# Optimization experiments

Hardware: AMD Instinct MI355X
Metric: run time of the kernel (lower is better)

The kernel has to match this reference:

```python
import jax, jax.numpy as jnp
import numpy as np

EMBED_DIM = 1024
NUM_HEADS = 16
HEAD_DIM = EMBED_DIM // NUM_HEADS


def setup_inputs() -> dict:
    key = jax.random.key(0)
    ks = jax.random.split(key, 5)
    B, N, D = 4, 2048, EMBED_DIM
    scale = 1.0 / np.sqrt(D)
    return {
        "x": jax.random.normal(ks[0], (B, N, D), dtype=jnp.float32),
        "w_qkv": jax.random.normal(ks[1], (D, 3 * D), dtype=jnp.float32) * scale,
        "b_qkv": jnp.zeros((3 * D,), dtype=jnp.float32),
        "w_proj": jax.random.normal(ks[2], (D, D), dtype=jnp.float32) * scale,
        "b_proj": jnp.zeros((D,), dtype=jnp.float32),
    }


def reference(x, w_qkv, b_qkv, w_proj, b_proj):
    B, N, D = x.shape
    H, Hd = NUM_HEADS, HEAD_DIM
    qkv = x @ w_qkv + b_qkv                      # [B, N, 3D]
    # 'b n (three h d) -> three b h n d'
    qkv = qkv.reshape(B, N, 3, H, Hd).transpose(2, 0, 3, 1, 4)
    q, k, v = qkv[0], qkv[1], qkv[2]             # each [B, H, N, Hd]
    scores = jnp.einsum('bhnd,bhmd->bhnm', q, k) / np.sqrt(Hd)
    probs = jax.nn.softmax(scores, axis=-1)      # dropout is identity in eval
    out = jnp.einsum('bhnm,bhmd->bhnd', probs, v)
    out = out.transpose(0, 2, 1, 3).reshape(B, N, D)  # 'b h n d -> b n (h d)'
    return out @ w_proj + b_proj
```

## Files before the change

kernel.cpp:

```cpp
#include <hip/hip_runtime.h>
#include <hip/hip_bf16.h>

#define DEVI __device__ __forceinline__

typedef float f32x4  __attribute__((ext_vector_type(4)));
typedef float f32x16 __attribute__((ext_vector_type(16)));
typedef short bf16x8 __attribute__((ext_vector_type(8)));
typedef int   i32x4  __attribute__((ext_vector_type(4)));

constexpr int BATCH = 4;
constexpr int SEQ   = 2048;
constexpr int DIM   = 1024;
constexpr int NH    = 16;
constexpr int HD    = 64;
constexpr int TD    = 3 * DIM;
constexpr int MTOT  = BATCH * SEQ;

constexpr float QSCALE = 0.125f * 1.44269504f;

DEVI unsigned short f2bf(float f) {
    __hip_bfloat16 h = __float2bfloat16(f);
    return *reinterpret_cast<unsigned short*>(&h);
}

DEVI void gload_lds16(const unsigned short* gsrc, unsigned short* ldst) {
    __builtin_amdgcn_global_load_lds(
        (const __attribute__((address_space(1))) void*)gsrc,
        (__attribute__((address_space(3))) void*)ldst,
        16, 0, 0);
}

__global__ void cvt_kernel(const float* __restrict__ in, unsigned short* __restrict__ out, int n4) {
    int i = blockIdx.x * blockDim.x + threadIdx.x;
    int stride = gridDim.x * blockDim.x;
    for (; i < n4; i += stride) {
        float4 v = reinterpret_cast<const float4*>(in)[i];
        ushort4 o;
        o.x = f2bf(v.x); o.y = f2bf(v.y); o.z = f2bf(v.z); o.w = f2bf(v.w);
        reinterpret_cast<ushort4*>(out)[i] = o;
    }
}

__global__ void transp_kernel(const float* __restrict__ in, unsigned short* __restrict__ out, int R, int C) {
    __shared__ float tile[32][33];
    int c0 = blockIdx.x * 32, r0 = blockIdx.y * 32;
    int tx = threadIdx.x, ty = threadIdx.y;
#pragma unroll
    for (int i = 0; i < 32; i += 8)
        tile[ty + i][tx] = in[(long)(r0 + ty + i) * C + c0 + tx];
    __syncthreads();
#pragma unroll
    for (int i = 0; i < 32; i += 8)
        out[(long)(c0 + ty + i) * R + r0 + tx] = f2bf(tile[tx][ty + i]);
}

template <bool OUT_BF16>
__global__ __launch_bounds__(256) void gemm_bt_kernel(
    const unsigned short* __restrict__ A,
    const unsigned short* __restrict__ Bt,
    const float* __restrict__ bias,
    void* __restrict__ Cout,
    int M, int Nn, int K, int scale_ncols, float scl)
{
    __shared__ unsigned short As[128 * 32];
    __shared__ unsigned short Bs[128 * 32];

    const int t  = threadIdx.x;
    const int l  = t & 63;
    const int w  = t >> 6;
    const int wr = w >> 1, wc = w & 1;
    const int tr = blockIdx.y, tc = blockIdx.x;
    const int lrow = l & 15, lk = l >> 4;

    f32x4 acc[4][4] = {};

    const int r0  = t >> 2;
    const int ch0 = t & 3;
    const long arow_base = (long)(tr * 128) * K;
    const long brow_base = (long)(tc * 128) * K;

    const int nk = K >> 5;
    for (int kt = 0; kt < nk; ++kt) {
        const int kb = kt * 32;
        gload_lds16(A  + arow_base + (long)r0 * K        + kb + ch0 * 8, &As[t * 8]);
        gload_lds16(A  + arow_base + (long)(r0 + 64) * K + kb + ch0 * 8, &As[(t + 256) * 8]);
        gload_lds16(Bt + brow_base + (long)r0 * K        + kb + ch0 * 8, &Bs[t * 8]);
        gload_lds16(Bt + brow_base + (long)(r0 + 64) * K + kb + ch0 * 8, &Bs[(t + 256) * 8]);
        __syncthreads();

        bf16x8 a[4], bb[4];
#pragma unroll
        for (int mi = 0; mi < 4; ++mi)
            a[mi] = *(const bf16x8*)&As[(wr * 64 + mi * 16 + lrow) * 32 + lk * 8];
#pragma unroll
        for (int ni = 0; ni < 4; ++ni)
            bb[ni] = *(const bf16x8*)&Bs[(wc * 64 + ni * 16 + lrow) * 32 + lk * 8];
#pragma unroll
        for (int mi = 0; mi < 4; ++mi)
#pragma unroll
            for (int ni = 0; ni < 4; ++ni)
                acc[mi][ni] = __builtin_amdgcn_mfma_f32_16x16x32_bf16(a[mi], bb[ni], acc[mi][ni], 0, 0, 0);
        __syncthreads();
    }

    const int row_base = tr * 128 + wr * 64;
    const int col_base = tc * 128 + wc * 64;
    const float mult = (col_base < scale_ncols) ? scl : 1.0f;
    float bv[4];
#pragma unroll
    for (int ni = 0; ni < 4; ++ni) bv[ni] = bias[col_base + ni * 16 + lrow];

#pragma unroll
    for (int mi = 0; mi < 4; ++mi)
#pragma unroll
        for (int ni = 0; ni < 4; ++ni)
#pragma unroll
            for (int r = 0; r < 4; ++r) {
                int row = row_base + mi * 16 + lk * 4 + r;
                int col = col_base + ni * 16 + lrow;
                float v = (acc[mi][ni][r] + bv[ni]) * mult;
                if (OUT_BF16) ((unsigned short*)Cout)[(long)row * Nn + col] = f2bf(v);
                else          ((float*)Cout)[(long)row * Nn + col] = v;
            }
}

__global__ __launch_bounds__(256, 2) void attn_kernel(
    const unsigned short* __restrict__ qkv,
    unsigned short* __restrict__ aout)
{
    constexpr int KVB  = 64;
    constexpr int PADW = 72;
    __shared__ unsigned short Ks[KVB * PADW];
    __shared__ unsigned short VsT[HD * PADW];

    const int t = threadIdx.x;
    const int l = t & 63;
    const int w = t >> 6;
    const int ln = l & 31;
    const int hi = l >> 5;

    const int b  = blockIdx.y >> 4;
    const int h  = blockIdx.y & 15;
    const int q0 = blockIdx.x * 128 + w * 32;

    bf16x8 bq[4];
    {
        const long qrow = (long)(b * SEQ + q0 + ln) * TD + h * HD;
#pragma unroll
        for (int s = 0; s < 4; ++s)
            bq[s] = *(const bf16x8*)&qkv[qrow + s * 16 + hi * 8];
    }

    f32x16 o[2];
#pragma unroll
    for (int i = 0; i < 16; ++i) { o[0][i] = 0.f; o[1][i] = 0.f; }
    float mrun = -1e30f, lsum = 0.f;

    const long kbase = (long)(b * SEQ) * TD + DIM + h * HD;
    const long vbase = (long)(b * SEQ) * TD + 2 * DIM + h * HD;

    const int krow = t & 63, kc0 = (t >> 6) * 8;
    const int vch = t >> 5, vrp = t & 31;

    i32x4 kr0, kr1, vr0, vr1;

#define LOAD_TILE(m0) do {                                                     \
        const unsigned short* kp = &qkv[kbase + (long)((m0) + krow) * TD + kc0]; \
        kr0 = *(const i32x4*)kp;                                               \
        kr1 = *(const i32x4*)(kp + 32);                                        \
        const unsigned short* vp = &qkv[vbase + (long)((m0) + 2 * vrp) * TD + vch * 8]; \
        vr0 = *(const i32x4*)vp;                                               \
        vr1 = *(const i32x4*)(vp + TD);                                        \
    } while (0)

#define WRITE_TILE() do {                                                      \
        *(i32x4*)&Ks[krow * PADW + kc0]      = kr0;                            \
        *(i32x4*)&Ks[krow * PADW + kc0 + 32] = kr1;                            \
        const unsigned short* u0 = (const unsigned short*)&vr0;                \
        const unsigned short* u1 = (const unsigned short*)&vr1;                \
        unsigned int* V32 = (unsigned int*)VsT;                                \
        _Pragma("unroll")                                                      \
        for (int j = 0; j < 8; ++j) {                                          \
            unsigned int word = (unsigned int)u0[j] | ((unsigned int)u1[j] << 16); \
            V32[(vch * 8 + j) * 36 + vrp] = word;                              \
        }                                                                      \
    } while (0)

    LOAD_TILE(0);
    WRITE_TILE();
    __syncthreads();

    for (int m0 = 0; m0 < SEQ; m0 += KVB) {
        const int mn = (m0 + KVB) & (SEQ - 1);
        LOAD_TILE(mn);

        f32x16 sv[2];
        __builtin_amdgcn_s_setprio(1);
#pragma unroll
        for (int f = 0; f < 2; ++f) {
            f32x16 acc = {};
#pragma unroll
            for (int s = 0; s < 4; ++s) {
                bf16x8 ak = *(const bf16x8*)&Ks[(f * 32 + ln) * PADW + s * 16 + hi * 8];
                acc = __builtin_amdgcn_mfma_f32_32x32x16_bf16(ak, bq[s], acc, 0, 0, 0);
            }
            sv[f] = acc;
        }
        __builtin_amdgcn_s_setprio(0);

        float vm = sv[0][0];
#pragma unroll
        for (int i = 1; i < 16; ++i) vm = fmaxf(vm, sv[0][i]);
#pragma unroll
        for (int i = 0; i < 16; ++i) vm = fmaxf(vm, sv[1][i]);
        vm = fmaxf(vm, __shfl_xor(vm, 32));

        if (!__all(vm <= mrun + 8.f)) {
            float mnew = fmaxf(mrun, vm);
            float sc = exp2f(mrun - mnew);
            mrun = mnew;
            lsum *= sc;
#pragma unroll
            for (int f = 0; f < 2; ++f)
#pragma unroll
                for (int i = 0; i < 16; ++i) o[f][i] *= sc;
        }

        float ps = 0.f;
#pragma unroll
        for (int f = 0; f < 2; ++f)
#pragma unroll
            for (int i = 0; i < 16; ++i) {
                float p = exp2f(sv[f][i] - mrun);
                sv[f][i] = p;
                ps += p;
            }
        ps += __shfl_xor(ps, 32);
        lsum += ps;

        bf16x8 pb[4];
#pragma unroll
        for (int ks = 0; ks < 4; ++ks) {
            const int f = ks >> 1, base = (ks & 1) * 8;
            unsigned x0, x1, y0, y1;
            asm("v_cvt_pk_bf16_f32 %0, %1, %2" : "=v"(x0) : "v"(sv[f][base + 0]), "v"(sv[f][base + 1]));
            asm("v_cvt_pk_bf16_f32 %0, %1, %2" : "=v"(x1) : "v"(sv[f][base + 2]), "v"(sv[f][base + 3]));
            asm("v_cvt_pk_bf16_f32 %0, %1, %2" : "=v"(y0) : "v"(sv[f][base + 4]), "v"(sv[f][base + 5]));
            asm("v_cvt_pk_bf16_f32 %0, %1, %2" : "=v"(y1) : "v"(sv[f][base + 6]), "v"(sv[f][base + 7]));
            asm("v_permlane32_swap_b32 %0, %1" : "+v"(x0), "+v"(y0));
            asm("v_permlane32_swap_b32 %0, %1" : "+v"(x1), "+v"(y1));
            union { unsigned u[4]; bf16x8 v; } pu;
            pu.u[0] = x0; pu.u[1] = x1; pu.u[2] = y0; pu.u[3] = y1;
            pb[ks] = pu.v;
        }

        __builtin_amdgcn_s_setprio(1);
#pragma unroll
        for (int f2 = 0; f2 < 2; ++f2)
#pragma unroll
            for (int ks = 0; ks < 4; ++ks) {
                bf16x8 av = *(const bf16x8*)&VsT[(f2 * 32 + ln) * PADW + ks * 16 + hi * 8];
                o[f2] = __builtin_amdgcn_mfma_f32_32x32x16_bf16(av, pb[ks], o[f2], 0, 0, 0);
            }
        __builtin_amdgcn_s_setprio(0);

        __syncthreads();
        WRITE_TILE();
        __syncthreads();
    }

#undef LOAD_TILE
#undef WRITE_TILE

    float inv = 1.0f / lsum;
    const long orow = (long)(b * SEQ + q0 + ln);
#pragma unroll
    for (int f2 = 0; f2 < 2; ++f2)
#pragma unroll
        for (int g = 0; g < 4; ++g) {
            ushort4 st;
            st.x = f2bf(o[f2][4 * g + 0] * inv);
            st.y = f2bf(o[f2][4 * g + 1] * inv);
            st.z = f2bf(o[f2][4 * g + 2] * inv);
            st.w = f2bf(o[f2][4 * g + 3] * inv);
            *(ushort4*)&aout[orow * DIM + h * HD + f2 * 32 + 8 * g + 4 * hi] = st;
        }
}

extern "C" void kernel_launch(void* const* d_in, const int* in_sizes, int n_in,
                              void* d_out, int out_size, void* d_ws, size_t ws_size,
                              hipStream_t stream)
{
    const float* x      = (const float*)d_in[0];
    const float* w_qkv  = (const float*)d_in[1];
    const float* b_qkv  = (const float*)d_in[2];
    const float* w_proj = (const float*)d_in[3];
    const float* b_proj = (const float*)d_in[4];
    float* out = (float*)d_out;

    unsigned short* x_bf   = (unsigned short*)d_ws;
    unsigned short* wqkvT  = x_bf   + (size_t)MTOT * DIM;
    unsigned short* wprojT = wqkvT  + (size_t)TD * DIM;
    unsigned short* qkv    = wprojT + (size_t)DIM * DIM;
    unsigned short* attn   = qkv    + (size_t)MTOT * TD;

    cvt_kernel<<<2048, 256, 0, stream>>>(x, x_bf, MTOT * DIM / 4);
    dim3 tb(32, 8);
    transp_kernel<<<dim3(TD / 32, DIM / 32), tb, 0, stream>>>(w_qkv, wqkvT, DIM, TD);
    transp_kernel<<<dim3(DIM / 32, DIM / 32), tb, 0, stream>>>(w_proj, wprojT, DIM, DIM);

    gemm_bt_kernel<true><<<dim3(TD / 128, MTOT / 128), 256, 0, stream>>>(
        x_bf, wqkvT, b_qkv, qkv, MTOT, TD, DIM, DIM, QSCALE);

    attn_kernel<<<dim3(SEQ / 128, BATCH * NH), 256, 0, stream>>>(qkv, attn);

    gemm_bt_kernel<false><<<dim3(DIM / 128, MTOT / 128), 256, 0, stream>>>(
        attn, wprojT, b_proj, out, MTOT, DIM, DIM, 0, 1.0f);
}
```

Measured before the change: 237.6 us.

## Double-buffer attention K/V tiles, swizzle blocks across XCDs, tree-reduce softmax

The attention kernel now uses two LDS buffers for K and V^T, so the next tile is written into the spare buffer and only one barrier per iteration is needed instead of two. Both the GEMM and attention kernels remap block indices so consecutive tiles land on the same XCD, which is meant to improve L2 reuse. The row max and row sum are rebuilt as balanced trees to shorten the dependency chains, and the attention kernel's min-2-blocks launch bound is dropped. Doubling LDS and relaxing the occupancy hint may lower occupancy. The attention swizzle hardcodes a 16x128 grid.

```diff
diff --git a/kernel.cpp b/kernel.cpp
--- a/kernel.cpp
+++ b/kernel.cpp
@@ -69,8 +69,15 @@
     const int l  = t & 63;
     const int w  = t >> 6;
     const int wr = w >> 1, wc = w & 1;
-    const int tr = blockIdx.y, tc = blockIdx.x;
     const int lrow = l & 15, lk = l >> 4;
+
+    const int gx  = gridDim.x;
+    const int nwg = gx * gridDim.y;
+    const int orig = blockIdx.y * gx + blockIdx.x;
+    const int xcd = orig & 7, idx = orig >> 3;
+    const int q8 = nwg >> 3, r8 = nwg & 7;
+    const int swz = (xcd < r8 ? xcd * (q8 + 1) : r8 * (q8 + 1) + (xcd - r8) * q8) + idx;
+    const int tr = swz / gx, tc = swz - tr * gx;
 
     f32x4 acc[4][4] = {};
 
@@ -124,14 +131,14 @@
             }
 }
 
-__global__ __launch_bounds__(256, 2) void attn_kernel(
+__global__ __launch_bounds__(256) void attn_kernel(
     const unsigned short* __restrict__ qkv,
     unsigned short* __restrict__ aout)
 {
     constexpr int KVB  = 64;
     constexpr int PADW = 72;
-    __shared__ unsigned short Ks[KVB * PADW];
-    __shared__ unsigned short VsT[HD * PADW];
+    __shared__ unsigned short Ks[2][KVB * PADW];
+    __shared__ unsigned short VsT[2][HD * PADW];
 
     const int t = threadIdx.x;
     const int l = t & 63;
@@ -139,9 +146,13 @@
     const int ln = l & 31;
     const int hi = l >> 5;
 
-    const int b  = blockIdx.y >> 4;
-    const int h  = blockIdx.y & 15;
-    const int q0 = blockIdx.x * 128 + w * 32;
+    const int orig = blockIdx.y * 16 + blockIdx.x;
+    const int swz  = (orig & 7) * 128 + (orig >> 3);
+    const int bx = swz & 15, by = swz >> 4;
+
+    const int b  = by >> 4;
+    const int h  = by & 15;
+    const int q0 = bx * 128 + w * 32;
 
     bf16x8 bq[4];
     {
@@ -173,12 +184,12 @@
         vr1 = *(const i32x4*)(vp + TD);                                        \
     } while (0)
 
-#define WRITE_TILE() do {                                                      \
-        *(i32x4*)&Ks[krow * PADW + kc0]      = kr0;                            \
-        *(i32x4*)&Ks[krow * PADW + kc0 + 32] = kr1;                            \
+#define WRITE_TILE(KD, VD) do {                                                \
+        *(i32x4*)&(KD)[krow * PADW + kc0]      = kr0;                          \
+        *(i32x4*)&(KD)[krow * PADW + kc0 + 32] = kr1;                          \
         const unsigned short* u0 = (const unsigned short*)&vr0;                \
         const unsigned short* u1 = (const unsigned short*)&vr1;                \
-        unsigned int* V32 = (unsigned int*)VsT;                                \
+        unsigned int* V32 = (unsigned int*)(VD);                               \
         _Pragma("unroll")                                                      \
         for (int j = 0; j < 8; ++j) {                                          \
             unsigned int word = (unsigned int)u0[j] | ((unsigned int)u1[j] << 16); \
@@ -187,13 +198,17 @@
     } while (0)
 
     LOAD_TILE(0);
-    WRITE_TILE();
+    WRITE_TILE(Ks[0], VsT[0]);
     __syncthreads();
 
+    int cur = 0;
     for (int m0 = 0; m0 < SEQ; m0 += KVB) {
         const int mn = (m0 + KVB) & (SEQ - 1);
         LOAD_TILE(mn);
 
+        const unsigned short* kcur = Ks[cur];
+        const unsigned short* vcur = VsT[cur];
+
         f32x16 sv[2];
         __builtin_amdgcn_s_setprio(1);
 #pragma unroll
@@ -201,18 +216,20 @@
             f32x16 acc = {};
 #pragma unroll
             for (int s = 0; s < 4; ++s) {
-                bf16x8 ak = *(const bf16x8*)&Ks[(f * 32 + ln) * PADW + s * 16 + hi * 8];
+                bf16x8 ak = *(const bf16x8*)&kcur[(f * 32 + ln) * PADW + s * 16 + hi * 8];
                 acc = __builtin_amdgcn_mfma_f32_32x32x16_bf16(ak, bq[s], acc, 0, 0, 0);
             }
             sv[f] = acc;
         }
         __builtin_amdgcn_s_setprio(0);
 
-        float vm = sv[0][0];
-#pragma unroll
-        for (int i = 1; i < 16; ++i) vm = fmaxf(vm, sv[0][i]);
-#pragma unroll
-        for (int i = 0; i < 16; ++i) vm = fmaxf(vm, sv[1][i]);
+        float m8[8];
+#pragma unroll
+        for (int i = 0; i < 8; ++i)
+            m8[i] = fmaxf(fmaxf(sv[0][i], sv[0][i + 8]), fmaxf(sv[1][i], sv[1][i + 8]));
+        float m4a = fmaxf(m8[0], m8[1]), m4b = fmaxf(m8[2], m8[3]);
+        float m4c = fmaxf(m8[4], m8[5]), m4d = fmaxf(m8[6], m8[7]);
+        float vm = fmaxf(fmaxf(m4a, m4b), fmaxf(m4c, m4d));
         vm = fmaxf(vm, __shfl_xor(vm, 32));
 
         if (!__all(vm <= mrun + 8.f)) {
@@ -226,17 +243,23 @@
                 for (int i = 0; i < 16; ++i) o[f][i] *= sc;
         }
 
-        float ps = 0.f;
 #pragma unroll
         for (int f = 0; f < 2; ++f)
 #pragma unroll
-            for (int i = 0; i < 16; ++i) {
-                float p = exp2f(sv[f][i] - mrun);
-                sv[f][i] = p;
-                ps += p;
-            }
-        ps += __shfl_xor(ps, 32);
-        lsum += ps;
+            for (int i = 0; i < 16; ++i)
+                sv[f][i] = exp2f(sv[f][i] - mrun);
+
+        {
+            float s8[8];
+#pragma unroll
+            for (int i = 0; i < 8; ++i)
+                s8[i] = (sv[0][i] + sv[0][i + 8]) + (sv[1][i] + sv[1][i + 8]);
+            float s4a = s8[0] + s8[1], s4b = s8[2] + s8[3];
+            float s4c = s8[4] + s8[5], s4d = s8[6] + s8[7];
+            float ps = (s4a + s4b) + (s4c + s4d);
+            ps += __shfl_xor(ps, 32);
+            lsum += ps;
+        }
 
         bf16x8 pb[4];
 #pragma unroll
@@ -259,14 +282,14 @@
         for (int f2 = 0; f2 < 2; ++f2)
 #pragma unroll
             for (int ks = 0; ks < 4; ++ks) {
-                bf16x8 av = *(const bf16x8*)&VsT[(f2 * 32 + ln) * PADW + ks * 16 + hi * 8];
+                bf16x8 av = *(const bf16x8*)&vcur[(f2 * 32 + ln) * PADW + ks * 16 + hi * 8];
                 o[f2] = __builtin_amdgcn_mfma_f32_32x32x16_bf16(av, pb[ks], o[f2], 0, 0, 0);
             }
         __builtin_amdgcn_s_setprio(0);
 
+        WRITE_TILE(Ks[cur ^ 1], VsT[cur ^ 1]);
         __syncthreads();
-        WRITE_TILE();
-        __syncthreads();
+        cur ^= 1;
     }
 
 #undef LOAD_TILE
```

Measured after the change: 247.8 us. +4.3%, slower.
